# Kernel tuning notes

Measured on AMD Instinct MI355X. Metric: run time of the kernel, lower is better.

## Reference

```python
import jax, jax.numpy as jnp
import numpy as np

B, DIM, L = 16, 1024, 1024
EPS = 1e-12  # F.normalize eps


def l2norm(x, axis=1):
    # torch F.normalize: x / clamp_min(||x||_2, eps)
    n = jnp.sqrt(jnp.sum(x * x, axis=axis, keepdims=True))
    return x / jnp.maximum(n, EPS)


def setup_inputs() -> dict:
    key = jax.random.key(0)
    ks = jax.random.split(key, 8)
    inp = {
        "V": jax.random.normal(ks[0], (B, DIM, L), dtype=jnp.float32),
        "T": jax.random.normal(ks[1], (B, DIM, L), dtype=jnp.float32),
    }
    scale = 1.0 / np.sqrt(DIM)
    names = ["WQ1", "WK1", "WV1", "Wq2", "Wk2", "Wv2"]
    for i, nme in enumerate(names):
        inp[nme] = jax.random.normal(ks[2 + i], (DIM, DIM), dtype=jnp.float32) * scale
    return inp


def reference(V, T, WQ1, WK1, WV1, Wq2, Wk2, Wv2):
    # V, T: [B, dim, L]
    T = l2norm(T, axis=1)                      # normalize over feature dim
    Vt = jnp.swapaxes(V, -2, -1)               # [B, L, dim]
    Tt = jnp.swapaxes(T, -2, -1)               # [B, L, dim]

    relu = jax.nn.relu
    q1 = relu(jnp.einsum('bld,ed->ble', Vt, WQ1))
    k1 = relu(jnp.einsum('bld,ed->ble', Tt, WK1))
    v1 = relu(jnp.einsum('bld,ed->ble', Tt, WV1))
    q2 = relu(jnp.einsum('bld,ed->ble', Tt, Wq2))
    k2 = relu(jnp.einsum('bld,ed->ble', Vt, Wk2))
    v2 = relu(jnp.einsum('bld,ed->ble', Vt, Wv2))

    inv_sqrt_d = 1.0 / jnp.sqrt(jnp.asarray(DIM, dtype=q1.dtype))

    s1 = jnp.einsum('bqd,bkd->bqk', q1, k1) * inv_sqrt_d   # [B, Lv, Lt]
    p1 = jax.nn.softmax(s1, axis=1)                        # softmax over query axis (dim=1)
    w1 = jnp.einsum('bqk,bkd->bqd', p1, v1)                # [B, Lv, dim]
    cV = l2norm(V + jnp.swapaxes(w1, -2, -1), axis=1)      # [B, dim, Lv]

    s2 = jnp.einsum('bqd,bkd->bqk', q2, k2) * inv_sqrt_d   # [B, Lt, Lv]
    p2 = jax.nn.softmax(s2, axis=1)
    w2 = jnp.einsum('bqk,bkd->bqd', p2, v2)                # [B, Lt, dim]
    cT = l2norm(T + jnp.swapaxes(w2, -2, -1), axis=1)      # [B, dim, Lt]

    return l2norm(cV + cT, axis=1)
```

## Files before the change

### kernel.cpp

```cpp
#include <hip/hip_runtime.h>

#define L 1024
#define DIM 1024
#define NB 16

typedef unsigned short u16;
typedef __attribute__((ext_vector_type(4))) float f32x4;
typedef __attribute__((ext_vector_type(8))) short s16x8;

__device__ __forceinline__ float bf2f(u16 x){
  union { unsigned u; float f; } c; c.u = ((unsigned)x) << 16; return c.f;
}
__device__ __forceinline__ u16 f2bf(float f){
  union { float f; unsigned u; } c; c.f = f;
  unsigned r = c.u + 0x7fffu + ((c.u >> 16) & 1u);
  return (u16)(r >> 16);
}
__device__ __forceinline__ void gload_lds16(const void* g, void* l){
  __builtin_amdgcn_global_load_lds(
      (const __attribute__((address_space(1))) void*)g,
      (__attribute__((address_space(3))) void*)l, 16, 0, 0);
}

struct WPtrs { const float* p[6]; };

__global__ __launch_bounds__(256) void k_wconv(WPtrs wp, u16* out){
  long idx = (long)blockIdx.x * blockDim.x + threadIdx.x;
  long base = idx * 4;
  int w = (int)(base >> 20);
  long off = base & ((1 << 20) - 1);
  float4 v = *(const float4*)(wp.p[w] + off);
  ushort4 o;
  o.x = f2bf(v.x); o.y = f2bf(v.y); o.z = f2bf(v.z); o.w = f2bf(v.w);
  *(ushort4*)(out + base) = o;
}

__global__ __launch_bounds__(256) void k_transpose(const float* X, u16* Xt, int bo){
  __shared__ u16 tile[64][68];
  int b = blockIdx.y;
  int d0 = (blockIdx.x >> 4) * 64;
  int l0 = (blockIdx.x & 15) * 64;
  const float* Xb = X + (long)(bo + b) * DIM * L;
  u16* Xtb = Xt + (long)b * L * DIM;
  int q = threadIdx.x & 15, g = threadIdx.x >> 4;
  for (int r = g; r < 64; r += 16){
    float4 v = *(const float4*)(Xb + (long)(d0 + r) * L + l0 + q * 4);
    ushort4 h; h.x = f2bf(v.x); h.y = f2bf(v.y); h.z = f2bf(v.z); h.w = f2bf(v.w);
    *(ushort4*)&tile[r][q * 4] = h;
  }
  __syncthreads();
  for (int r = g; r < 64; r += 16){
    ushort4 h;
    h.x = tile[q * 4 + 0][r]; h.y = tile[q * 4 + 1][r];
    h.z = tile[q * 4 + 2][r]; h.w = tile[q * 4 + 3][r];
    *(ushort4*)&Xtb[(long)(l0 + r) * DIM + d0 + q * 4] = h;
  }
}

__global__ __launch_bounds__(256) void k_tnorm(const float* T_, u16* Tnt, float* rT, int bo){
  __shared__ float red[16][16][5];
  __shared__ float rn[64];
  __shared__ u16 tile[64][68];
  int b = blockIdx.y; int l0 = blockIdx.x * 64;
  const float* Tb = T_ + (long)(bo + b) * DIM * L;
  int q = threadIdx.x & 15, g = threadIdx.x >> 4;
  f32x4 ss = {0.f, 0.f, 0.f, 0.f};
  for (int d = g; d < DIM; d += 16){
    float4 v = *(const float4*)(Tb + (long)d * L + l0 + q * 4);
    f32x4 vv = {v.x, v.y, v.z, v.w};
    ss += vv * vv;
  }
  #pragma unroll
  for (int e = 0; e < 4; e++) red[g][q][e] = ss[e];
  __syncthreads();
  if (threadIdx.x < 64){
    int c = threadIdx.x;
    float n = 0.f;
    #pragma unroll
    for (int gg = 0; gg < 16; gg++) n += red[gg][c >> 2][c & 3];
    float r = 1.0f / fmaxf(sqrtf(n), 1e-12f);
    rn[c] = r;
    rT[(long)b * L + l0 + c] = r;
  }
  __syncthreads();
  float r0 = rn[q * 4], r1 = rn[q * 4 + 1], r2 = rn[q * 4 + 2], r3 = rn[q * 4 + 3];
  u16* Tntb = Tnt + (long)b * L * DIM;
  for (int ch = 0; ch < 16; ch++){
    int dbase = ch * 64;
    for (int r = g; r < 64; r += 16){
      float4 v = *(const float4*)(Tb + (long)(dbase + r) * L + l0 + q * 4);
      ushort4 h;
      h.x = f2bf(v.x * r0); h.y = f2bf(v.y * r1);
      h.z = f2bf(v.z * r2); h.w = f2bf(v.w * r3);
      *(ushort4*)&tile[r][q * 4] = h;
    }
    __syncthreads();
    for (int r = g; r < 64; r += 16){
      ushort4 h;
      h.x = tile[q * 4 + 0][r]; h.y = tile[q * 4 + 1][r];
      h.z = tile[q * 4 + 2][r]; h.w = tile[q * 4 + 3][r];
      *(ushort4*)&Tntb[(long)(l0 + r) * DIM + dbase + q * 4] = h;
    }
    __syncthreads();
  }
}


struct GemmDesc {
  const u16* A[4]; const u16* B[4]; u16* C[4];
  long sA[4], sB[4], sC[4];
  int epi[4];
  float scale;
};

#define PH(slot, mq, nq, LA, LB, STAGE, WAITC) do {                           \
  if (LA){                                                                    \
    _Pragma("unroll")                                                         \
    for (int f = 0; f < 4; f++){                                              \
      av[f][0] = *(const s16x8*)&lds[(slot)*16384 + arow + (mq)*4096 + f*1024 + cko0]; \
      av[f][1] = *(const s16x8*)&lds[(slot)*16384 + arow + (mq)*4096 + f*1024 + cko1]; \
    }                                                                         \
  }                                                                           \
  if (LB){                                                                    \
    _Pragma("unroll")                                                         \
    for (int g2 = 0; g2 < 2; g2++){                                           \
      bv[nq][g2][0] = *(const s16x8*)&lds[32768 + (slot)*16384 + brow + (nq)*2048 + g2*1024 + cko0]; \
      bv[nq][g2][1] = *(const s16x8*)&lds[32768 + (slot)*16384 + brow + (nq)*2048 + g2*1024 + cko1]; \
    }                                                                         \
  }                                                                           \
  STAGE;                                                                      \
  WAITC;                                                                      \
  __builtin_amdgcn_s_barrier();                                               \
  asm volatile("s_waitcnt lgkmcnt(0)" ::: "memory");                          \
  __builtin_amdgcn_sched_barrier(0);                                          \
  __builtin_amdgcn_s_setprio(1);                                              \
  _Pragma("unroll")                                                           \
  for (int f = 0; f < 4; f++)                                                 \
    _Pragma("unroll")                                                         \
    for (int g2 = 0; g2 < 2; g2++){                                           \
      acc[(mq)*4+f][(nq)*2+g2] = __builtin_amdgcn_mfma_f32_16x16x32_bf16(     \
          av[f][0], bv[nq][g2][0], acc[(mq)*4+f][(nq)*2+g2], 0, 0, 0);        \
      acc[(mq)*4+f][(nq)*2+g2] = __builtin_amdgcn_mfma_f32_16x16x32_bf16(     \
          av[f][1], bv[nq][g2][1], acc[(mq)*4+f][(nq)*2+g2], 0, 0, 0);        \
    }                                                                         \
  __builtin_amdgcn_s_setprio(0);                                              \
  __builtin_amdgcn_s_barrier();                                               \
} while(0)

__global__ __launch_bounds__(512, 2) void k_gemmM(GemmDesc gd, int shift){
  constexpr int K = 1024, NN = 1024, NT = K / 64, NIT = NT / 2;
  __shared__ u16 lds[65536];

  int tid = threadIdx.x;
  int w = tid >> 6, l = tid & 63;
  int wr = w >> 2, wc = w & 3;
  int lr = l & 15, cb = l >> 4;

  int nwg = gridDim.x, cpx = nwg >> 3;
  int swz = (blockIdx.x & 7) * cpx + (blockIdx.x >> 3);
  int mat = swz >> shift;
  int local = swz & ((1 << shift) - 1);
  int batch = local >> 4;
  int tile = local & 15;
  int bm = (tile >> 2) * 256, bn = (tile & 3) * 256;

  const u16* Ab = gd.A[mat] + (long)batch * gd.sA[mat] + (long)bm * K;
  const u16* Bb = gd.B[mat] + (long)batch * gd.sB[mat] + (long)bn * K;
  int epi = gd.epi[mat];

  int arow = (wr * 128 + lr) * 64;
  int brow = (wc * 64 + lr) * 64;
  int cko0 = ((cb) ^ (lr & 7)) * 8;
  int cko1 = ((4 + cb) ^ (lr & 7)) * 8;

  int srow8 = l >> 3;
  int schunk = (l & 7) ^ (l >> 3);

  auto stA = [&](int slot, int t, int q){
    #pragma unroll
    for (int j = 0; j < 2; j++){
      int wb = w * 2 + j;
      int gr = ((wb >> 3) * 128) + ((wb & 7) * 8) + q * 64;
      gload_lds16(Ab + (long)(gr + srow8) * K + t * 64 + schunk * 8,
                  (u16*)lds + slot * 16384 + gr * 64);
    }
  };
  auto stB = [&](int slot, int t, int q){
    #pragma unroll
    for (int j = 0; j < 2; j++){
      int wb = w * 2 + j;
      int gr = ((wb >> 2) * 64) + ((wb & 3) * 8) + q * 32;
      gload_lds16(Bb + (long)(gr + srow8) * K + t * 64 + schunk * 8,
                  (u16*)lds + 32768 + slot * 16384 + gr * 64);
    }
  };

  f32x4 acc[8][4] = {};
  s16x8 av[4][2];
  s16x8 bv[2][2][2];

  stA(0, 0, 0); stB(0, 0, 0); stA(0, 0, 1); stB(0, 0, 1);
  stA(1, 1, 0); stB(1, 1, 0);
  asm volatile("s_waitcnt vmcnt(4)" ::: "memory");
  __builtin_amdgcn_s_barrier();

  #pragma unroll 1
  for (int i = 0; i < NIT - 1; ++i){
    int t1 = 2 * i + 1, t2 = 2 * i + 2, t3 = 2 * i + 3;
    PH(0, 0, 0, 1, 1, stA(1, t1, 1), (void)0);
    PH(0, 0, 1, 0, 1, stB(1, t1, 1), (void)0);
    PH(0, 1, 0, 1, 0, stA(0, t2, 0), (void)0);
    PH(0, 1, 1, 0, 0, stB(0, t2, 0), asm volatile("s_waitcnt vmcnt(4)" ::: "memory"));
    PH(1, 0, 0, 1, 1, stA(0, t2, 1), (void)0);
    PH(1, 0, 1, 0, 1, stB(0, t2, 1), (void)0);
    PH(1, 1, 0, 1, 0, stA(1, t3, 0), (void)0);
    PH(1, 1, 1, 0, 0, stB(1, t3, 0), asm volatile("s_waitcnt vmcnt(4)" ::: "memory"));
  }
  {
    int t1 = NT - 1;
    PH(0, 0, 0, 1, 1, stA(1, t1, 1), (void)0);
    PH(0, 0, 1, 0, 1, stB(1, t1, 1), (void)0);
    PH(0, 1, 0, 1, 0, (void)0, (void)0);
    PH(0, 1, 1, 0, 0, (void)0, asm volatile("s_waitcnt vmcnt(0)" ::: "memory"));
    PH(1, 0, 0, 1, 1, (void)0, (void)0);
    PH(1, 0, 1, 0, 1, (void)0, (void)0);
    PH(1, 1, 0, 1, 0, (void)0, (void)0);
    PH(1, 1, 1, 0, 0, (void)0, (void)0);
  }

  u16* Cb = gd.C[mat] + (long)batch * gd.sC[mat];
  float sc = gd.scale;
  int cb4 = cb * 4;
  #pragma unroll
  for (int ai = 0; ai < 8; ai++)
    #pragma unroll
    for (int j = 0; j < 4; j++)
      #pragma unroll
      for (int r = 0; r < 4; r++){
        float v = acc[ai][j][r];
        if (epi == 0) v = fmaxf(v, 0.f);
        else if (epi == 1) v = __expf(v * sc);
        int row = bm + wr * 128 + ai * 16 + cb4 + r;
        int col = bn + wc * 64 + j * 16 + lr;
        Cb[(long)row * NN + col] = f2bf(v);
      }
}

__global__ __launch_bounds__(256) void k_colzs(const u16* E1, const u16* E2,
                                               u16* v1, u16* v2){
  __shared__ float red[32][8][9];
  __shared__ float invs[64];
  int side = blockIdx.x >> 4;
  int k0 = (blockIdx.x & 15) * 64;
  int b = blockIdx.y;
  const u16* Eb = (side ? E2 : E1) + (long)b * L * L + k0;
  u16* vb = (side ? v2 : v1) + (long)b * L * DIM + k0;
  int co = threadIdx.x & 7, g = threadIdx.x >> 3;
  float z[8] = {0.f, 0.f, 0.f, 0.f, 0.f, 0.f, 0.f, 0.f};
  for (int qq = g; qq < L; qq += 32){
    s16x8 h = *(const s16x8*)(Eb + (long)qq * L + co * 8);
    #pragma unroll
    for (int e = 0; e < 8; e++) z[e] += bf2f((u16)h[e]);
  }
  #pragma unroll
  for (int e = 0; e < 8; e++) red[g][co][e] = z[e];
  __syncthreads();
  if (threadIdx.x < 64){
    int c = threadIdx.x;
    float s = 0.f;
    #pragma unroll
    for (int gg = 0; gg < 32; gg++) s += red[gg][c >> 3][c & 7];
    invs[c] = 1.0f / s;
  }
  __syncthreads();
  float iz[8];
  #pragma unroll
  for (int e = 0; e < 8; e++) iz[e] = invs[co * 8 + e];
  for (int r = g; r < DIM; r += 32){
    s16x8 h = *(const s16x8*)(vb + (long)r * L + co * 8);
    s16x8 o;
    #pragma unroll
    for (int e = 0; e < 8; e++) o[e] = (short)f2bf(bf2f((u16)h[e]) * iz[e]);
    *(s16x8*)(vb + (long)r * L + co * 8) = o;
  }
}

__global__ __launch_bounds__(1024) void k_final(const float* V, const float* T_,
                                                const float* rT, const u16* w1t,
                                                const u16* w2t, float* out, int bo){
  __shared__ float red[64][16][13];
  __shared__ float fac[3][64];
  int b = blockIdx.y;
  int c0 = blockIdx.x * 64;
  long gbase = (long)(bo + b) * DIM * L + c0;
  long lbase = (long)b * DIM * L + c0;
  int cq = threadIdx.x & 15, g = threadIdx.x >> 4;
  int coff = cq * 4;
  float4 rt4 = *(const float4*)(rT + (long)b * L + c0 + coff);
  f32x4 rtv = {rt4.x, rt4.y, rt4.z, rt4.w};
  f32x4 s1 = {0.f,0.f,0.f,0.f}, s2 = {0.f,0.f,0.f,0.f}, s12 = {0.f,0.f,0.f,0.f};
  #pragma unroll 4
  for (int d = g; d < DIM; d += 64){
    long o = (long)d * L + coff;
    float4 v = *(const float4*)(V + gbase + o);
    float4 t = *(const float4*)(T_ + gbase + o);
    ushort4 w1 = *(const ushort4*)(w1t + lbase + o);
    ushort4 w2 = *(const ushort4*)(w2t + lbase + o);
    f32x4 a = {v.x + bf2f(w1.x), v.y + bf2f(w1.y), v.z + bf2f(w1.z), v.w + bf2f(w1.w)};
    f32x4 tt = {t.x, t.y, t.z, t.w};
    f32x4 bb = tt * rtv;
    bb[0] += bf2f(w2.x); bb[1] += bf2f(w2.y); bb[2] += bf2f(w2.z); bb[3] += bf2f(w2.w);
    s1 += a * a; s2 += bb * bb; s12 += a * bb;
  }
  #pragma unroll
  for (int e = 0; e < 4; e++){
    red[g][cq][e] = s1[e];
    red[g][cq][4 + e] = s2[e];
    red[g][cq][8 + e] = s12[e];
  }
  __syncthreads();
  if (threadIdx.x < 192){
    int q = threadIdx.x / 12, s = threadIdx.x % 12;
    float acc = 0.f;
    #pragma unroll 8
    for (int gg = 0; gg < 64; gg++) acc += red[gg][q][s];
    red[0][q][s] = acc;
  }
  __syncthreads();
  if (threadIdx.x < 64){
    int c = threadIdx.x;
    float n1 = red[0][c >> 2][c & 3];
    float n2 = red[0][c >> 2][4 + (c & 3)];
    float cc = red[0][c >> 2][8 + (c & 3)];
    float rn1 = 1.f / fmaxf(sqrtf(n1), 1e-12f);
    float rn2 = 1.f / fmaxf(sqrtf(n2), 1e-12f);
    float n3 = n1 * rn1 * rn1 + 2.f * cc * rn1 * rn2 + n2 * rn2 * rn2;
    float rn3 = 1.f / fmaxf(sqrtf(n3), 1e-12f);
    fac[0][c] = rn1; fac[1][c] = rn2; fac[2][c] = rn3;
  }
  __syncthreads();
  f32x4 f1, f2, f3;
  #pragma unroll
  for (int e = 0; e < 4; e++){
    f1[e] = fac[0][coff + e]; f2[e] = fac[1][coff + e]; f3[e] = fac[2][coff + e];
  }
  #pragma unroll 4
  for (int d = g; d < DIM; d += 64){
    long o = (long)d * L + coff;
    float4 v = *(const float4*)(V + gbase + o);
    float4 t = *(const float4*)(T_ + gbase + o);
    ushort4 w1 = *(const ushort4*)(w1t + lbase + o);
    ushort4 w2 = *(const ushort4*)(w2t + lbase + o);
    f32x4 a = {v.x + bf2f(w1.x), v.y + bf2f(w1.y), v.z + bf2f(w1.z), v.w + bf2f(w1.w)};
    f32x4 tt = {t.x, t.y, t.z, t.w};
    f32x4 bb = tt * rtv;
    bb[0] += bf2f(w2.x); bb[1] += bf2f(w2.y); bb[2] += bf2f(w2.z); bb[3] += bf2f(w2.w);
    f32x4 r = (a * f1 + bb * f2) * f3;
    float4 st = {r[0], r[1], r[2], r[3]};
    *(float4*)(out + gbase + o) = st;
  }
}

extern "C" void kernel_launch(void* const* d_in, const int* in_sizes, int n_in,
                              void* d_out, int out_size, void* d_ws, size_t ws_size,
                              hipStream_t stream) {
  const float* V = (const float*)d_in[0];
  const float* T = (const float*)d_in[1];
  char* ws = (char*)d_ws;
  const long MB = 1 << 20;
  float* out = (float*)d_out;

  int G = NB;
  while (G > 1 && (size_t)((13 + 14 * (long)G) * MB) > ws_size) G >>= 1;
  int shift = 4 + (31 - __builtin_clz((unsigned)G));

  u16*   Wb  = (u16*)(ws);
  float* rT  = (float*)(ws + 12 * MB);
  char*  bufs = ws + 13 * MB;
  long   BUF  = (long)G * 2 * MB;
  u16* S0 = (u16*)(bufs + 0 * BUF);
  u16* S1 = (u16*)(bufs + 1 * BUF);
  u16* S2 = (u16*)(bufs + 2 * BUF);
  u16* S3 = (u16*)(bufs + 3 * BUF);
  u16* S4 = (u16*)(bufs + 4 * BUF);
  u16* S5 = (u16*)(bufs + 5 * BUF);
  u16* S6 = (u16*)(bufs + 6 * BUF);

  WPtrs wp;
  for (int i = 0; i < 6; i++) wp.p[i] = (const float*)d_in[2 + i];
  const u16* WQ1 = Wb + 0L * MB; const u16* WK1 = Wb + 1L * MB;
  const u16* WV1 = Wb + 2L * MB; const u16* Wq2 = Wb + 3L * MB;
  const u16* Wk2 = Wb + 4L * MB; const u16* Wv2 = Wb + 5L * MB;

  long LD = (long)L * DIM;
  const float invsq = 0.03125f;

  u16* Vt = S0, *Tnt = S1;
  u16* k1 = S2, *v1 = S3, *q2 = S4;
  u16* q1 = S5, *k2 = S6, *v2 = S1;
  u16* E1 = S0, *E2 = S5;
  u16* w1b = S2, *w2b = S4;

  GemmDesc g1 = {};
  g1.A[0] = Tnt; g1.B[0] = WK1; g1.C[0] = k1; g1.sA[0] = LD; g1.sB[0] = 0;  g1.sC[0] = LD;
  g1.A[1] = WV1; g1.B[1] = Tnt; g1.C[1] = v1; g1.sA[1] = 0;  g1.sB[1] = LD; g1.sC[1] = LD;
  g1.A[2] = Tnt; g1.B[2] = Wq2; g1.C[2] = q2; g1.sA[2] = LD; g1.sB[2] = 0;  g1.sC[2] = LD;
  g1.epi[0] = g1.epi[1] = g1.epi[2] = 0; g1.scale = 0.f;
  g1.A[3] = Tnt; g1.B[3] = WK1; g1.C[3] = k1; g1.sA[3] = LD; g1.sB[3] = 0; g1.sC[3] = LD; g1.epi[3] = 0;

  GemmDesc g2 = {};
  g2.A[0] = Vt;  g2.B[0] = WQ1; g2.C[0] = q1; g2.sA[0] = LD; g2.sB[0] = 0;  g2.sC[0] = LD;
  g2.A[1] = Vt;  g2.B[1] = Wk2; g2.C[1] = k2; g2.sA[1] = LD; g2.sB[1] = 0;  g2.sC[1] = LD;
  g2.A[2] = Wv2; g2.B[2] = Vt;  g2.C[2] = v2; g2.sA[2] = 0;  g2.sB[2] = LD; g2.sC[2] = LD;
  g2.epi[0] = g2.epi[1] = g2.epi[2] = 0; g2.scale = 0.f;
  g2.A[3] = Vt; g2.B[3] = WQ1; g2.C[3] = q1; g2.sA[3] = LD; g2.sB[3] = 0; g2.sC[3] = LD; g2.epi[3] = 0;

  GemmDesc g3a = {};
  g3a.A[0] = q1; g3a.B[0] = k1; g3a.C[0] = E1;
  g3a.sA[0] = LD; g3a.sB[0] = LD; g3a.sC[0] = LD; g3a.epi[0] = 1; g3a.scale = invsq;
  for (int i = 1; i < 4; i++){ g3a.A[i] = q1; g3a.B[i] = k1; g3a.C[i] = E1;
    g3a.sA[i] = LD; g3a.sB[i] = LD; g3a.sC[i] = LD; g3a.epi[i] = 1; }

  GemmDesc g3b = g3a;
  for (int i = 0; i < 4; i++){ g3b.A[i] = q2; g3b.B[i] = k2; g3b.C[i] = E2; }

  GemmDesc g4 = {};
  g4.A[0] = v1; g4.B[0] = E1; g4.C[0] = w1b;
  g4.A[1] = v2; g4.B[1] = E2; g4.C[1] = w2b;
  g4.A[2] = v1; g4.B[2] = E1; g4.C[2] = w1b;
  g4.A[3] = v1; g4.B[3] = E1; g4.C[3] = w1b;
  for (int i = 0; i < 4; i++){ g4.sA[i] = LD; g4.sB[i] = LD; g4.sC[i] = LD; g4.epi[i] = 3; }
  g4.scale = 0.f;

  k_wconv<<<6144, 256, 0, stream>>>(wp, Wb);

  for (int bo = 0; bo < NB; bo += G){
    k_transpose<<<dim3(256, G), 256, 0, stream>>>(V, Vt, bo);
    k_tnorm<<<dim3(16, G), 256, 0, stream>>>(T, Tnt, rT, bo);

    k_gemmM<<<3 * 16 * G, 512, 0, stream>>>(g1, shift);
    k_gemmM<<<3 * 16 * G, 512, 0, stream>>>(g2, shift);
    k_gemmM<<<1 * 16 * G, 512, 0, stream>>>(g3a, shift);
    k_gemmM<<<1 * 16 * G, 512, 0, stream>>>(g3b, shift);
    k_colzs<<<dim3(32, G), 256, 0, stream>>>(E1, E2, v1, v2);
    k_gemmM<<<2 * 16 * G, 512, 0, stream>>>(g4, shift);

    k_final<<<dim3(16, G), 1024, 0, stream>>>(V, T, rT, w1b, w2b, out, bo);
  }
}
```

Before: 591.4 us.

## Fuse softmax column sums into score GEMM epilogue and fold normalization into V projection

The separate column-sum/normalize kernel is removed. The exp-score GEMM epilogue now accumulates per-column sums with warp shuffles and atomics into Z buffers, and the V projections move after the score GEMMs so their epilogue applies ReLU and the reciprocal column sum directly. Q/K projections are merged into one 4-matrix launch, buffers are remapped, and the vmcnt wait counts in the GEMM pipeline are loosened (waits of 6/8 instead of 4). Risks are atomic contention and nondeterministic summation order, plus possible hazards from the relaxed wait counts.

```diff
diff --git a/kernel.cpp b/kernel.cpp
--- a/kernel.cpp
+++ b/kernel.cpp
@@ -57,13 +57,18 @@
   }
 }
 
-__global__ __launch_bounds__(256) void k_tnorm(const float* T_, u16* Tnt, float* rT, int bo){
+__global__ __launch_bounds__(256) void k_tnorm(const float* T_, u16* Tnt, float* rT,
+                                               float* Z1, float* Z2, int bo){
   __shared__ float red[16][16][5];
   __shared__ float rn[64];
   __shared__ u16 tile[64][68];
   int b = blockIdx.y; int l0 = blockIdx.x * 64;
   const float* Tb = T_ + (long)(bo + b) * DIM * L;
   int q = threadIdx.x & 15, g = threadIdx.x >> 4;
+  if (threadIdx.x < 64){
+    Z1[(long)b * L + l0 + threadIdx.x] = 0.f;
+    Z2[(long)b * L + l0 + threadIdx.x] = 0.f;
+  }
   f32x4 ss = {0.f, 0.f, 0.f, 0.f};
   for (int d = g; d < DIM; d += 16){
     float4 v = *(const float4*)(Tb + (long)d * L + l0 + q * 4);
@@ -108,10 +113,16 @@
 
 struct GemmDesc {
   const u16* A[4]; const u16* B[4]; u16* C[4];
+  float* Z[4];
   long sA[4], sB[4], sC[4];
   int epi[4];
   float scale;
 };
+
+#define VM6 asm volatile("s_waitcnt vmcnt(6)" ::: "memory")
+#define VM8 asm volatile("s_waitcnt vmcnt(8)" ::: "memory")
+#define VM4 asm volatile("s_waitcnt vmcnt(4)" ::: "memory")
+#define VM0 asm volatile("s_waitcnt vmcnt(0)" ::: "memory")
 
 #define PH(slot, mq, nq, LA, LB, STAGE, WAITC) do {                           \
   if (LA){                                                                    \
@@ -201,28 +212,28 @@
 
   stA(0, 0, 0); stB(0, 0, 0); stA(0, 0, 1); stB(0, 0, 1);
   stA(1, 1, 0); stB(1, 1, 0);
-  asm volatile("s_waitcnt vmcnt(4)" ::: "memory");
+  VM8;
   __builtin_amdgcn_s_barrier();
 
   #pragma unroll 1
   for (int i = 0; i < NIT - 1; ++i){
     int t1 = 2 * i + 1, t2 = 2 * i + 2, t3 = 2 * i + 3;
-    PH(0, 0, 0, 1, 1, stA(1, t1, 1), (void)0);
+    PH(0, 0, 0, 1, 1, stA(1, t1, 1), VM6);
     PH(0, 0, 1, 0, 1, stB(1, t1, 1), (void)0);
     PH(0, 1, 0, 1, 0, stA(0, t2, 0), (void)0);
-    PH(0, 1, 1, 0, 0, stB(0, t2, 0), asm volatile("s_waitcnt vmcnt(4)" ::: "memory"));
-    PH(1, 0, 0, 1, 1, stA(0, t2, 1), (void)0);
+    PH(0, 1, 1, 0, 0, stB(0, t2, 0), VM8);
+    PH(1, 0, 0, 1, 1, stA(0, t2, 1), VM6);
     PH(1, 0, 1, 0, 1, stB(0, t2, 1), (void)0);
     PH(1, 1, 0, 1, 0, stA(1, t3, 0), (void)0);
-    PH(1, 1, 1, 0, 0, stB(1, t3, 0), asm volatile("s_waitcnt vmcnt(4)" ::: "memory"));
+    PH(1, 1, 1, 0, 0, stB(1, t3, 0), VM8);
   }
   {
     int t1 = NT - 1;
-    PH(0, 0, 0, 1, 1, stA(1, t1, 1), (void)0);
+    PH(0, 0, 0, 1, 1, stA(1, t1, 1), VM6);
     PH(0, 0, 1, 0, 1, stB(1, t1, 1), (void)0);
     PH(0, 1, 0, 1, 0, (void)0, (void)0);
-    PH(0, 1, 1, 0, 0, (void)0, asm volatile("s_waitcnt vmcnt(0)" ::: "memory"));
-    PH(1, 0, 0, 1, 1, (void)0, (void)0);
+    PH(0, 1, 1, 0, 0, (void)0, VM4);
+    PH(1, 0, 0, 1, 1, (void)0, VM0);
     PH(1, 0, 1, 0, 1, (void)0, (void)0);
     PH(1, 1, 0, 1, 0, (void)0, (void)0);
     PH(1, 1, 1, 0, 0, (void)0, (void)0);
@@ -230,6 +241,13 @@
 
   u16* Cb = gd.C[mat] + (long)batch * gd.sC[mat];
   float sc = gd.scale;
+  float iz[4];
+  if (epi == 2){
+    const float* Zp = gd.Z[mat] + (long)batch * NN;
+    #pragma unroll
+    for (int j = 0; j < 4; j++) iz[j] = 1.0f / Zp[bn + wc * 64 + j * 16 + lr];
+  }
+  float cs[4] = {0.f, 0.f, 0.f, 0.f};
   int cb4 = cb * 4;
   #pragma unroll
   for (int ai = 0; ai < 8; ai++)
@@ -239,49 +257,21 @@
       for (int r = 0; r < 4; r++){
         float v = acc[ai][j][r];
         if (epi == 0) v = fmaxf(v, 0.f);
-        else if (epi == 1) v = __expf(v * sc);
+        else if (epi == 1){ v = __expf(v * sc); cs[j] += v; }
+        else if (epi == 2) v = fmaxf(v, 0.f) * iz[j];
         int row = bm + wr * 128 + ai * 16 + cb4 + r;
         int col = bn + wc * 64 + j * 16 + lr;
         Cb[(long)row * NN + col] = f2bf(v);
       }
-}
-
-__global__ __launch_bounds__(256) void k_colzs(const u16* E1, const u16* E2,
-                                               u16* v1, u16* v2){
-  __shared__ float red[32][8][9];
-  __shared__ float invs[64];
-  int side = blockIdx.x >> 4;
-  int k0 = (blockIdx.x & 15) * 64;
-  int b = blockIdx.y;
-  const u16* Eb = (side ? E2 : E1) + (long)b * L * L + k0;
-  u16* vb = (side ? v2 : v1) + (long)b * L * DIM + k0;
-  int co = threadIdx.x & 7, g = threadIdx.x >> 3;
-  float z[8] = {0.f, 0.f, 0.f, 0.f, 0.f, 0.f, 0.f, 0.f};
-  for (int qq = g; qq < L; qq += 32){
-    s16x8 h = *(const s16x8*)(Eb + (long)qq * L + co * 8);
-    #pragma unroll
-    for (int e = 0; e < 8; e++) z[e] += bf2f((u16)h[e]);
-  }
-  #pragma unroll
-  for (int e = 0; e < 8; e++) red[g][co][e] = z[e];
-  __syncthreads();
-  if (threadIdx.x < 64){
-    int c = threadIdx.x;
-    float s = 0.f;
-    #pragma unroll
-    for (int gg = 0; gg < 32; gg++) s += red[gg][c >> 3][c & 7];
-    invs[c] = 1.0f / s;
-  }
-  __syncthreads();
-  float iz[8];
-  #pragma unroll
-  for (int e = 0; e < 8; e++) iz[e] = invs[co * 8 + e];
-  for (int r = g; r < DIM; r += 32){
-    s16x8 h = *(const s16x8*)(vb + (long)r * L + co * 8);
-    s16x8 o;
-    #pragma unroll
-    for (int e = 0; e < 8; e++) o[e] = (short)f2bf(bf2f((u16)h[e]) * iz[e]);
-    *(s16x8*)(vb + (long)r * L + co * 8) = o;
+  if (epi == 1){
+    float* Zp = gd.Z[mat] + (long)batch * NN;
+    #pragma unroll
+    for (int j = 0; j < 4; j++){
+      float c = cs[j];
+      c += __shfl_xor(c, 16);
+      c += __shfl_xor(c, 32);
+      if (l < 16) atomicAdd(&Zp[bn + wc * 64 + j * 16 + l], c);
+    }
   }
 }
 
@@ -376,6 +366,8 @@
 
   u16*   Wb  = (u16*)(ws);
   float* rT  = (float*)(ws + 12 * MB);
+  float* Z1  = (float*)(ws + 12 * MB + 128 * 1024);
+  float* Z2  = (float*)(ws + 12 * MB + 256 * 1024);
   char*  bufs = ws + 13 * MB;
   long   BUF  = (long)G * 2 * MB;
   u16* S0 = (u16*)(bufs + 0 * BUF);
@@ -396,39 +388,43 @@
   const float invsq = 0.03125f;
 
   u16* Vt = S0, *Tnt = S1;
-  u16* k1 = S2, *v1 = S3, *q2 = S4;
-  u16* q1 = S5, *k2 = S6, *v2 = S1;
-  u16* E1 = S0, *E2 = S5;
-  u16* w1b = S2, *w2b = S4;
+  u16* k1 = S2, *q2 = S3, *q1 = S4, *k2 = S5;
+  u16* E1 = S6, *E2 = S4;
+  u16* v1 = S2, *v2 = S5;
+  u16* w1b = S3, *w2b = S0;
 
   GemmDesc g1 = {};
-  g1.A[0] = Tnt; g1.B[0] = WK1; g1.C[0] = k1; g1.sA[0] = LD; g1.sB[0] = 0;  g1.sC[0] = LD;
-  g1.A[1] = WV1; g1.B[1] = Tnt; g1.C[1] = v1; g1.sA[1] = 0;  g1.sB[1] = LD; g1.sC[1] = LD;
-  g1.A[2] = Tnt; g1.B[2] = Wq2; g1.C[2] = q2; g1.sA[2] = LD; g1.sB[2] = 0;  g1.sC[2] = LD;
-  g1.epi[0] = g1.epi[1] = g1.epi[2] = 0; g1.scale = 0.f;
-  g1.A[3] = Tnt; g1.B[3] = WK1; g1.C[3] = k1; g1.sA[3] = LD; g1.sB[3] = 0; g1.sC[3] = LD; g1.epi[3] = 0;
-
-  GemmDesc g2 = {};
-  g2.A[0] = Vt;  g2.B[0] = WQ1; g2.C[0] = q1; g2.sA[0] = LD; g2.sB[0] = 0;  g2.sC[0] = LD;
-  g2.A[1] = Vt;  g2.B[1] = Wk2; g2.C[1] = k2; g2.sA[1] = LD; g2.sB[1] = 0;  g2.sC[1] = LD;
-  g2.A[2] = Wv2; g2.B[2] = Vt;  g2.C[2] = v2; g2.sA[2] = 0;  g2.sB[2] = LD; g2.sC[2] = LD;
-  g2.epi[0] = g2.epi[1] = g2.epi[2] = 0; g2.scale = 0.f;
-  g2.A[3] = Vt; g2.B[3] = WQ1; g2.C[3] = q1; g2.sA[3] = LD; g2.sB[3] = 0; g2.sC[3] = LD; g2.epi[3] = 0;
+  g1.A[0] = Vt;  g1.B[0] = WQ1; g1.C[0] = q1;
+  g1.A[1] = Tnt; g1.B[1] = WK1; g1.C[1] = k1;
+  g1.A[2] = Tnt; g1.B[2] = Wq2; g1.C[2] = q2;
+  g1.A[3] = Vt;  g1.B[3] = Wk2; g1.C[3] = k2;
+  for (int i = 0; i < 4; i++){ g1.sA[i] = LD; g1.sB[i] = 0; g1.sC[i] = LD;
+    g1.epi[i] = 0; g1.Z[i] = Z1; }
+  g1.scale = 0.f;
 
   GemmDesc g3a = {};
-  g3a.A[0] = q1; g3a.B[0] = k1; g3a.C[0] = E1;
-  g3a.sA[0] = LD; g3a.sB[0] = LD; g3a.sC[0] = LD; g3a.epi[0] = 1; g3a.scale = invsq;
-  for (int i = 1; i < 4; i++){ g3a.A[i] = q1; g3a.B[i] = k1; g3a.C[i] = E1;
-    g3a.sA[i] = LD; g3a.sB[i] = LD; g3a.sC[i] = LD; g3a.epi[i] = 1; }
-
-  GemmDesc g3b = g3a;
-  for (int i = 0; i < 4; i++){ g3b.A[i] = q2; g3b.B[i] = k2; g3b.C[i] = E2; }
+  for (int i = 0; i < 4; i++){ g3a.A[i] = q1; g3a.B[i] = k1; g3a.C[i] = E1;
+    g3a.sA[i] = LD; g3a.sB[i] = LD; g3a.sC[i] = LD; g3a.epi[i] = 1; g3a.Z[i] = Z1; }
+  g3a.scale = invsq;
+
+  GemmDesc g3b = {};
+  for (int i = 0; i < 4; i++){ g3b.A[i] = q2; g3b.B[i] = k2; g3b.C[i] = E2;
+    g3b.sA[i] = LD; g3b.sB[i] = LD; g3b.sC[i] = LD; g3b.epi[i] = 1; g3b.Z[i] = Z2; }
+  g3b.scale = invsq;
+
+  GemmDesc gv = {};
+  gv.A[0] = WV1; gv.B[0] = Tnt; gv.C[0] = v1; gv.Z[0] = Z1;
+  gv.A[1] = Wv2; gv.B[1] = Vt;  gv.C[1] = v2; gv.Z[1] = Z2;
+  gv.A[2] = WV1; gv.B[2] = Tnt; gv.C[2] = v1; gv.Z[2] = Z1;
+  gv.A[3] = WV1; gv.B[3] = Tnt; gv.C[3] = v1; gv.Z[3] = Z1;
+  for (int i = 0; i < 4; i++){ gv.sA[i] = 0; gv.sB[i] = LD; gv.sC[i] = LD; gv.epi[i] = 2; }
+  gv.scale = 0.f;
 
   GemmDesc g4 = {};
-  g4.A[0] = v1; g4.B[0] = E1; g4.C[0] = w1b;
-  g4.A[1] = v2; g4.B[1] = E2; g4.C[1] = w2b;
-  g4.A[2] = v1; g4.B[2] = E1; g4.C[2] = w1b;
-  g4.A[3] = v1; g4.B[3] = E1; g4.C[3] = w1b;
+  g4.A[0] = v1; g4.B[0] = E1; g4.C[0] = w1b; g4.Z[0] = Z1;
+  g4.A[1] = v2; g4.B[1] = E2; g4.C[1] = w2b; g4.Z[1] = Z2;
+  g4.A[2] = v1; g4.B[2] = E1; g4.C[2] = w1b; g4.Z[2] = Z1;
+  g4.A[3] = v1; g4.B[3] = E1; g4.C[3] = w1b; g4.Z[3] = Z1;
   for (int i = 0; i < 4; i++){ g4.sA[i] = LD; g4.sB[i] = LD; g4.sC[i] = LD; g4.epi[i] = 3; }
   g4.scale = 0.f;
 
@@ -436,13 +432,12 @@
 
   for (int bo = 0; bo < NB; bo += G){
     k_transpose<<<dim3(256, G), 256, 0, stream>>>(V, Vt, bo);
-    k_tnorm<<<dim3(16, G), 256, 0, stream>>>(T, Tnt, rT, bo);
-
-    k_gemmM<<<3 * 16 * G, 512, 0, stream>>>(g1, shift);
-    k_gemmM<<<3 * 16 * G, 512, 0, stream>>>(g2, shift);
+    k_tnorm<<<dim3(16, G), 256, 0, stream>>>(T, Tnt, rT, Z1, Z2, bo);
+
+    k_gemmM<<<4 * 16 * G, 512, 0, stream>>>(g1, shift);
     k_gemmM<<<1 * 16 * G, 512, 0, stream>>>(g3a, shift);
     k_gemmM<<<1 * 16 * G, 512, 0, stream>>>(g3b, shift);
-    k_colzs<<<dim3(32, G), 256, 0, stream>>>(E1, E2, v1, v2);
+    k_gemmM<<<2 * 16 * G, 512, 0, stream>>>(gv, shift);
     k_gemmM<<<2 * 16 * G, 512, 0, stream>>>(g4, shift);
 
     k_final<<<dim3(16, G), 1024, 0, stream>>>(V, T, rT, w1b, w2b, out, bo);
```

Measured after the change: 582.7 us. No clear change (-1.5%).
